# Optimization experiments

Measured on AMD Instinct MI355X. Metric: run time of the kernel, lower is better.

Reference implementation:

```python
import jax, jax.numpy as jnp
import numpy as np

B, H, S, D = 2048, 1024, 32768, 64  # batch, hidden_dim, memory_slots, slot_size


def setup_inputs() -> dict:
    key = jax.random.key(0)
    ks = jax.random.split(key, 8)
    inp = {
        "query": jax.random.normal(ks[0], (B, H), jnp.float32),
        "consciousness_level": jax.random.uniform(ks[1], (B,), jnp.float32),
        "content": jax.random.normal(ks[2], (B, H), jnp.float32),
        "memory": jax.random.normal(ks[3], (S, D), jnp.float32) * 0.1,
        "memory_age": jnp.zeros((S,), jnp.float32),
        "memory_strength": jnp.ones((S,), jnp.float32) * 0.1,
        "W_read": jax.random.normal(ks[4], (H + 1, S), jnp.float32) / np.sqrt(H + 1),
        "b_read": jnp.zeros((S,), jnp.float32),
        "W_write": jax.random.normal(ks[5], (H + 1, S), jnp.float32) / np.sqrt(H + 1),
        "b_write": jnp.zeros((S,), jnp.float32),
        "W_cp": jax.random.normal(ks[6], (H, D), jnp.float32) / np.sqrt(H),
        "b_cp": jnp.zeros((D,), jnp.float32),
        "W_ce": jax.random.normal(ks[7], (D, H), jnp.float32) / np.sqrt(D),
        "b_ce": jnp.zeros((H,), jnp.float32),
    }
    return inp


def reference(query, consciousness_level, content, memory, memory_age,
              memory_strength, W_read, b_read, W_write, b_write,
              W_cp, b_cp, W_ce, b_ce):
    # ---- read path ----
    enhanced_query = jnp.concatenate([query, consciousness_level[:, None]], axis=-1)  # [B, H+1]
    read_weights = jax.nn.softmax(enhanced_query @ W_read + b_read, axis=-1)          # [B, S]
    boosted = read_weights * memory_strength[None, :]
    boosted = boosted / (boosted.sum(axis=-1, keepdims=True) + 1e-6)
    read_content = boosted @ memory                                                   # [B, D]
    consciousness_boost = read_content @ W_ce + b_ce                                  # [B, H]

    # ---- write path (vectorized masked consolidation over all slots) ----
    c_mean = consciousness_level.mean()
    write_weights = jax.nn.softmax(enhanced_query @ W_write + b_write, axis=-1)       # [B, S]
    ww_mean = write_weights.mean(axis=0)                                              # [S]
    pc_mean = (content @ W_cp + b_cp).mean(axis=0)                                    # [D]
    weight = ww_mean * (c_mean * 2.0)                                                 # [S]
    gate = c_mean >= 0.3                                                              # auto-activation threshold
    mask = (weight > 0.005) & gate                                                    # [S] bool
    consolidation = jax.nn.sigmoid(memory_age * 0.1 + c_mean)                         # [S]
    alpha = weight * consolidation                                                    # [S]
    new_memory = jnp.where(mask[:, None],
                           (1.0 - alpha)[:, None] * memory + alpha[:, None] * pc_mean[None, :],
                           memory)                                                    # [S, D]
    new_age = memory_age + mask.astype(memory_age.dtype)
    new_strength = jnp.where(mask,
                             jnp.clip(memory_strength + weight * 0.1, 0.1, 2.0),
                             memory_strength)
    return read_content, consciousness_boost, new_memory, new_age, new_strength
```

## Files before the change

### kernel.cpp

```cpp
#include <hip/hip_runtime.h>
#include <hip/hip_bf16.h>
#include <cstdint>
#include <cstddef>

#define B_ 2048
#define H_ 1024
#define S_ 32768
#define D_ 64
#define BT 32
#define KP 1088
#define NT 17

typedef unsigned short u16;
typedef __attribute__((ext_vector_type(8))) short bf16x8;
typedef __attribute__((ext_vector_type(4))) float f32x4;
typedef __attribute__((ext_vector_type(8))) unsigned short ushort8v;

#define WS_CMEAN      0
#define WS_PCMEAN     64
#define WS_ZERO_BEGIN 128
#define WS_CMM        128
#define WS_ZR         (WS_CMM + H_)
#define WS_TR         (WS_ZR + B_)
#define WS_VR         (WS_TR + B_)
#define WS_ZW         (WS_VR + B_*D_)
#define WS_WWM        (WS_ZW + B_)
#define WS_END        (WS_WWM + S_)

__device__ __forceinline__ u16 f2bf(float f) {
  unsigned u = __float_as_uint(f);
  unsigned r = (u + 0x7FFFu + ((u >> 16) & 1u)) >> 16;
  return (u16)r;
}

__device__ __forceinline__ void gload_lds16(const void* g, void* l) {
  __builtin_amdgcn_global_load_lds(
      (const __attribute__((address_space(1))) unsigned int*)g,
      (__attribute__((address_space(3))) unsigned int*)l, 16, 0, 0);
}

__global__ void k_stats(const float* __restrict__ content,
                        const float* __restrict__ cl, float* __restrict__ ws) {
  const int gx = blockIdx.x, gy = blockIdx.y, t = threadIdx.x;
  if (gx < 4) {
    const int h = gx * 256 + t;
    const int b0 = gy * 256;
    float acc = 0.f;
    #pragma unroll 8
    for (int b = 0; b < 256; ++b) acc += content[(size_t)(b0 + b) * H_ + h];
    atomicAdd(&ws[WS_CMM + h], acc * (1.0f / B_));
  } else if (gy == 0) {
    float acc = 0.f;
    for (int i = t; i < B_; i += 256) acc += cl[i];
    #pragma unroll
    for (int off = 32; off > 0; off >>= 1) acc += __shfl_down(acc, off);
    __shared__ float red[4];
    if ((t & 63) == 0) red[t >> 6] = acc;
    __syncthreads();
    if (t == 0) ws[WS_CMEAN] = (red[0] + red[1] + red[2] + red[3]) * (1.0f / B_);
  }
}

__global__ void k_pcmean(const float* __restrict__ Wcp, const float* __restrict__ bcp,
                         float* __restrict__ ws) {
  const int d = threadIdx.x;
  const float* __restrict__ cmm = &ws[WS_CMM];
  float acc = bcp[d];
  #pragma unroll 4
  for (int k = 0; k < H_; ++k) acc = fmaf(cmm[k], Wcp[(size_t)k * D_ + d], acc);
  ws[WS_PCMEAN + d] = acc;
}


__global__ void k_cvt_q(const float* __restrict__ query, const float* __restrict__ cl,
                        u16* __restrict__ qb) {
  const int b = blockIdx.x, t = threadIdx.x;
  const float c = cl[b];
  #pragma unroll
  for (int i = 0; i < 5; ++i) {
    const int k = i * 256 + t;
    if (k < KP) {
      float v;
      if (k < H_) v = query[(size_t)b * H_ + k];
      else if (k == H_) v = c;
      else if (k == H_ + 1) v = 1.0f;
      else v = 0.f;
      qb[(size_t)b * KP + k] = f2bf(v);
    }
  }
}

__global__ void k_cvt_wt(const float* __restrict__ W, const float* __restrict__ bias,
                         u16* __restrict__ wbt) {
  __shared__ float tile[64][65];
  const int t = threadIdx.x;
  const int s0 = blockIdx.x * 64;
  const int k0 = blockIdx.y * 64;
  const int c = t & 63, rbase = t >> 6;
  #pragma unroll
  for (int i = 0; i < 16; ++i) {
    const int r = rbase + i * 4;
    const int k = k0 + r;
    float v = 0.f;
    if (k <= H_) v = W[(size_t)k * S_ + s0 + c];
    else if (k == H_ + 1) v = bias[s0 + c];
    tile[r][c] = v;
  }
  __syncthreads();
  #pragma unroll
  for (int i = 0; i < 16; ++i) {
    const int sr = rbase + i * 4;
    const int k = k0 + c;
    if (k < KP) wbt[(size_t)(s0 + sr) * KP + k] = f2bf(tile[c][sr]);
  }
}

__global__ void k_cvt_memT(const float* __restrict__ mem, u16* __restrict__ mT) {
  __shared__ float tile[64][65];
  const int t = threadIdx.x;
  const int s0 = blockIdx.x * 64;
  const int c = t & 63, rbase = t >> 6;
  #pragma unroll
  for (int i = 0; i < 16; ++i) {
    const int r = rbase + i * 4;
    tile[r][c] = mem[(size_t)(s0 + r) * D_ + c];
  }
  __syncthreads();
  #pragma unroll
  for (int i = 0; i < 16; ++i) {
    const int d = rbase + i * 4;
    mT[(size_t)d * S_ + s0 + c] = f2bf(tile[c][d]);
  }
}

template <int NF>
__device__ __forceinline__ void rd_frags(const u16* __restrict__ lds, int rowbase,
                                         int lr, int lg, bf16x8 (&dst)[NF * 2]) {
  #pragma unroll
  for (int f = 0; f < NF; ++f) {
    const int rr = rowbase + f * 16 + lr;
    #pragma unroll
    for (int ks = 0; ks < 2; ++ks) {
      const int ch = (ks * 4 + lg) ^ (rr & 7);
      dst[f * 2 + ks] = *(const bf16x8*)&lds[rr * 64 + ch * 8];
    }
  }
}

template <int QR, int QC>
__device__ __forceinline__ void mfmaq(f32x4 (&acc)[8][4], const bf16x8 (&av)[8],
                                      const bf16x8 (&bv)[4]) {
  #pragma unroll
  for (int m16 = 0; m16 < 4; ++m16)
    #pragma unroll
    for (int n16 = 0; n16 < 2; ++n16)
      #pragma unroll
      for (int ks = 0; ks < 2; ++ks)
        acc[QR * 4 + m16][QC * 2 + n16] = __builtin_amdgcn_mfma_f32_16x16x32_bf16(
            av[m16 * 2 + ks], bv[n16 * 2 + ks], acc[QR * 4 + m16][QC * 2 + n16], 0, 0, 0);
}

template <int VARIANT>
__global__ __launch_bounds__(512, 2) void k_gemm(
    const u16* __restrict__ qb, const u16* __restrict__ wbt,
    const float* __restrict__ strength,
    u16* __restrict__ pout, float* __restrict__ ws) {
  __shared__ __align__(16) u16 Ab[2][256 * 64];
  __shared__ __align__(16) u16 Bb[2][256 * 64];
  const int t = threadIdx.x;
  const int w = t >> 6, l = t & 63;
  const int wm = w >> 2, wn = w & 3;
  const int lr = l & 15, lg = l >> 4;

  const int lin = blockIdx.x + 8 * blockIdx.y;
  const int xcd = lin & 7, idx = lin >> 3;
  const size_t r0 = (size_t)(idx & 7) * 256;
  const size_t c0 = (size_t)(xcd * 16 + (idx >> 3)) * 256;

  f32x4 acc[8][4];
  #pragma unroll
  for (int m = 0; m < 8; ++m)
    #pragma unroll
    for (int n = 0; n < 4; ++n) acc[m][n] = (f32x4)0.f;

  auto STAGE = [&](int kt2, int pp) {
    #pragma unroll
    for (int i = 0; i < 4; ++i) {
      const int q = i * 512 + t;
      const int r = q >> 3;
      const int sc = (q & 7) ^ (r & 7);
      gload_lds16(qb + (r0 + r) * KP + (size_t)kt2 * 64 + sc * 8, &Ab[pp][q * 8]);
    }
    #pragma unroll
    for (int i = 0; i < 4; ++i) {
      const int q = i * 512 + t;
      const int r = q >> 3;
      const int sc = (q & 7) ^ (r & 7);
      gload_lds16(wbt + (c0 + r) * KP + (size_t)kt2 * 64 + sc * 8, &Bb[pp][q * 8]);
    }
  };

  STAGE(0, 0);
  STAGE(1, 1);
  asm volatile("s_waitcnt vmcnt(8)" ::: "memory");
  __builtin_amdgcn_sched_barrier(0);
  __builtin_amdgcn_s_barrier();

  for (int kt = 0; kt < NT; ++kt) {
    const int p = kt & 1;
    const u16* __restrict__ Ap = &Ab[p][0];
    const u16* __restrict__ Bp = &Bb[p][0];
    bf16x8 a[8], b0[4], b1[4];
    rd_frags<4>(Ap, wm * 128 + 0, lr, lg, a);
    rd_frags<2>(Bp, wn * 64 + 0, lr, lg, b0);
    __builtin_amdgcn_sched_barrier(0);
    __builtin_amdgcn_s_barrier();
    __builtin_amdgcn_s_setprio(1);
    mfmaq<0, 0>(acc, a, b0);
    __builtin_amdgcn_s_setprio(0);
    __builtin_amdgcn_s_barrier();
    rd_frags<2>(Bp, wn * 64 + 32, lr, lg, b1);
    __builtin_amdgcn_sched_barrier(0);
    __builtin_amdgcn_s_barrier();
    __builtin_amdgcn_s_setprio(1);
    mfmaq<0, 1>(acc, a, b1);
    __builtin_amdgcn_s_setprio(0);
    __builtin_amdgcn_s_barrier();
    rd_frags<4>(Ap, wm * 128 + 64, lr, lg, a);
    __builtin_amdgcn_sched_barrier(0);
    __builtin_amdgcn_s_barrier();
    __builtin_amdgcn_s_setprio(1);
    mfmaq<1, 1>(acc, a, b1);
    __builtin_amdgcn_s_setprio(0);
    __builtin_amdgcn_s_barrier();
    if (kt + 2 < NT) STAGE(kt + 2, p);
    __builtin_amdgcn_s_barrier();
    __builtin_amdgcn_s_setprio(1);
    mfmaq<1, 0>(acc, a, b0);
    __builtin_amdgcn_s_setprio(0);
    if (kt + 2 < NT) {
      asm volatile("s_waitcnt vmcnt(8)" ::: "memory");
    } else if (kt + 1 < NT) {
      asm volatile("s_waitcnt vmcnt(0)" ::: "memory");
    }
    __builtin_amdgcn_sched_barrier(0);
    __builtin_amdgcn_s_barrier();
  }

  float* zred = (float*)&Ab[0][0];
  float* tred = zred + 256;
  if (t < 512) zred[t] = 0.f;
  __syncthreads();

  float st4[4];
  if (VARIANT == 0) {
    #pragma unroll
    for (int n = 0; n < 4; ++n) st4[n] = strength[c0 + wn * 64 + n * 16 + lr];
  }
  #pragma unroll
  for (int m = 0; m < 8; ++m) {
    #pragma unroll
    for (int j = 0; j < 4; ++j) {
      const int rloc = wm * 128 + m * 16 + lg * 4 + j;
      const size_t R = r0 + rloc;
      float ze = 0.f, zp = 0.f;
      u16 pb[4];
      #pragma unroll
      for (int n = 0; n < 4; ++n) {
        const float e = __expf(acc[m][n][j]);
        const float pv = (VARIANT == 0) ? e * st4[n] : e;
        ze += e;
        zp += pv;
        pb[n] = f2bf(pv);
      }
      #pragma unroll
      for (int n = 0; n < 4; ++n)
        pout[R * S_ + c0 + wn * 64 + n * 16 + lr] = pb[n];
      #pragma unroll
      for (int off = 1; off < 16; off <<= 1) {
        ze += __shfl_xor(ze, off);
        if (VARIANT == 0) zp += __shfl_xor(zp, off);
      }
      if (lr == 0) {
        atomicAdd(&zred[rloc], ze);
        if (VARIANT == 0) atomicAdd(&tred[rloc], zp);
      }
    }
  }
  __syncthreads();
  if (t < 256) {
    if (VARIANT == 0) {
      atomicAdd(&ws[WS_ZR + r0 + t], zred[t]);
      atomicAdd(&ws[WS_TR + r0 + t], tred[t]);
    } else {
      atomicAdd(&ws[WS_ZW + r0 + t], zred[t]);
    }
  }
}

__global__ void k_pv(const u16* __restrict__ P, const u16* __restrict__ mT,
                     float* __restrict__ ws) {
  __shared__ float Vs[64 * 64];
  const int t = threadIdx.x;
  const int w = t >> 6, l = t & 63;
  const int lr = l & 15, lg = l >> 4;
  const size_t r0 = (size_t)blockIdx.x * 64;
  const size_t s0 = (size_t)blockIdx.y * 1024 + (size_t)w * 256;
  f32x4 acc[4][4];
  #pragma unroll
  for (int m = 0; m < 4; ++m)
    #pragma unroll
    for (int n = 0; n < 4; ++n) acc[m][n] = (f32x4)0.f;

  for (int ks = 0; ks < 8; ++ks) {
    const size_t sb = s0 + ks * 32 + lg * 8;
    bf16x8 a[4], b[4];
    #pragma unroll
    for (int m = 0; m < 4; ++m)
      a[m] = *(const bf16x8*)&P[(r0 + m * 16 + lr) * S_ + sb];
    #pragma unroll
    for (int n = 0; n < 4; ++n)
      b[n] = *(const bf16x8*)&mT[(size_t)(n * 16 + lr) * S_ + sb];
    #pragma unroll
    for (int m = 0; m < 4; ++m)
      #pragma unroll
      for (int n = 0; n < 4; ++n)
        acc[m][n] = __builtin_amdgcn_mfma_f32_16x16x32_bf16(a[m], b[n], acc[m][n], 0, 0, 0);
  }
  for (int i = t; i < 4096; i += 256) Vs[i] = 0.f;
  __syncthreads();
  #pragma unroll
  for (int m = 0; m < 4; ++m)
    #pragma unroll
    for (int j = 0; j < 4; ++j)
      #pragma unroll
      for (int n = 0; n < 4; ++n)
        atomicAdd(&Vs[(m * 16 + lg * 4 + j) * 64 + n * 16 + lr], acc[m][n][j]);
  __syncthreads();
  for (int i = t; i < 4096; i += 256)
    atomicAdd(&ws[WS_VR + (r0 + (size_t)(i >> 6)) * 64 + (i & 63)], Vs[i]);
}


__global__ void k_wwm_store(const __hip_bfloat16* __restrict__ ebuf,
                            float* __restrict__ ws) {
  const int t = threadIdx.x;
  const int s0 = blockIdx.x * 2048 + t * 8;
  const int b0 = blockIdx.y * 128;
  const u16* __restrict__ eb = (const u16*)ebuf;
  float ww[8];
  #pragma unroll
  for (int j = 0; j < 8; ++j) ww[j] = 0.f;
  #pragma unroll 1
  for (int b = 0; b < 128; ++b) {
    const float inv = 1.0f / ws[WS_ZW + b0 + b];
    const ushort8v ev = *reinterpret_cast<const ushort8v*>(&eb[(size_t)(b0 + b) * S_ + s0]);
    #pragma unroll
    for (int j = 0; j < 8; ++j) {
      const float e = __uint_as_float(((unsigned)ev[j]) << 16);
      ww[j] = fmaf(e, inv, ww[j]);
    }
  }
  #pragma unroll
  for (int j = 0; j < 8; ++j) atomicAdd(&ws[WS_WWM + s0 + j], ww[j]);
}

__global__ void k_rc(const float* __restrict__ ws, float* __restrict__ out) {
  const int idx = blockIdx.x * 256 + threadIdx.x;
  const int b = idx >> 6;
  const float z = ws[WS_ZR + b], tt = ws[WS_TR + b];
  out[idx] = ws[WS_VR + idx] / (tt + 1e-6f * z);
}

__global__ void k_cboost(const float* __restrict__ rc, const float* __restrict__ Wce,
                         const float* __restrict__ bce, float* __restrict__ out) {
  const int idx = blockIdx.x * 256 + threadIdx.x;
  const int b = idx >> 10, h = idx & 1023;
  const float* __restrict__ rcb = &rc[b * 64];
  float acc = bce[h];
  #pragma unroll
  for (int dd = 0; dd < 64; dd += 4) {
    const float4 r4 = *reinterpret_cast<const float4*>(&rcb[dd]);
    acc = fmaf(r4.x, Wce[(size_t)(dd + 0) * H_ + h], acc);
    acc = fmaf(r4.y, Wce[(size_t)(dd + 1) * H_ + h], acc);
    acc = fmaf(r4.z, Wce[(size_t)(dd + 2) * H_ + h], acc);
    acc = fmaf(r4.w, Wce[(size_t)(dd + 3) * H_ + h], acc);
  }
  out[idx] = acc;
}

__global__ void k_final(const float* __restrict__ mem, const float* __restrict__ age,
                        const float* __restrict__ strength, const float* __restrict__ ws,
                        float* __restrict__ out_mem, float* __restrict__ out_age,
                        float* __restrict__ out_str) {
  const int idx = blockIdx.x * 256 + threadIdx.x;
  const int s = idx >> 6, dd = idx & 63;
  const float cm = ws[WS_CMEAN];
  const float w = ws[WS_WWM + s] * (2.0f * cm / B_);
  const bool mask = (w > 0.005f) && (cm >= 0.3f);
  float m = mem[idx];
  if (mask) {
    const float cons = 1.0f / (1.0f + __expf(-(age[s] * 0.1f + cm)));
    const float alpha = w * cons;
    m = (1.0f - alpha) * m + alpha * ws[WS_PCMEAN + dd];
  }
  out_mem[idx] = m;
  if (dd == 0) {
    out_age[s] = age[s] + (mask ? 1.0f : 0.0f);
    out_str[s] = mask ? fminf(fmaxf(strength[s] + w * 0.1f, 0.1f), 2.0f) : strength[s];
  }
}


template <int NR>
__device__ __forceinline__ void logits_kloop(const float* __restrict__ q, int row0,
                                             const float* __restrict__ W, int s,
                                             float* acc) {
  #pragma unroll 1
  for (int k = 0; k < H_; k += 4) {
    const float w0 = W[(size_t)(k + 0) * S_ + s];
    const float w1 = W[(size_t)(k + 1) * S_ + s];
    const float w2 = W[(size_t)(k + 2) * S_ + s];
    const float w3 = W[(size_t)(k + 3) * S_ + s];
    #pragma unroll
    for (int r = 0; r < NR; ++r) {
      const float4 qv = *reinterpret_cast<const float4*>(&q[(size_t)(row0 + r) * H_ + k]);
      float a = acc[r];
      a = fmaf(qv.x, w0, a);
      a = fmaf(qv.y, w1, a);
      a = fmaf(qv.z, w2, a);
      a = fmaf(qv.w, w3, a);
      acc[r] = a;
    }
  }
}

__global__ __launch_bounds__(512, 2) void k_read(
    const float* __restrict__ q, const float* __restrict__ cl,
    const float* __restrict__ Wr, const float* __restrict__ br,
    const float* __restrict__ strength, const float* __restrict__ mem,
    float* __restrict__ ws) {
  __shared__ float plds[BT * 512];
  const int t = threadIdx.x;
  const int r0 = blockIdx.x * BT;
  const int squar = blockIdx.y;
  const int d = t & 63, wv = t >> 6;

  float zacc[BT], tacc[BT];
  #pragma unroll
  for (int r = 0; r < BT; ++r) { zacc[r] = 0.f; tacc[r] = 0.f; }
  float vacc[4] = {0.f, 0.f, 0.f, 0.f};

  for (int tile = 0; tile < 16; ++tile) {
    const int sg0 = squar * 8192 + tile * 512;
    const int s = sg0 + t;
    float acc[BT];
    const float wlast = Wr[(size_t)H_ * S_ + s];
    const float bias = br[s];
    #pragma unroll
    for (int r = 0; r < BT; ++r) acc[r] = fmaf(cl[r0 + r], wlast, bias);
    logits_kloop<BT>(q, r0, Wr, s, acc);

    const float stg = strength[s];
    #pragma unroll
    for (int r = 0; r < BT; ++r) {
      const float e = __expf(acc[r]);
      zacc[r] += e;
      const float p = e * stg;
      tacc[r] += p;
      plds[r * 512 + t] = p;
    }
    __syncthreads();
    #pragma unroll 1
    for (int sl = 0; sl < 512; sl += 4) {
      const float m0 = mem[(size_t)(sg0 + sl + 0) * D_ + d];
      const float m1 = mem[(size_t)(sg0 + sl + 1) * D_ + d];
      const float m2 = mem[(size_t)(sg0 + sl + 2) * D_ + d];
      const float m3 = mem[(size_t)(sg0 + sl + 3) * D_ + d];
      #pragma unroll
      for (int j = 0; j < 4; ++j) {
        const float4 pv = *reinterpret_cast<const float4*>(&plds[(wv + 8 * j) * 512 + sl]);
        float v = vacc[j];
        v = fmaf(pv.x, m0, v);
        v = fmaf(pv.y, m1, v);
        v = fmaf(pv.z, m2, v);
        v = fmaf(pv.w, m3, v);
        vacc[j] = v;
      }
    }
    __syncthreads();
  }

  float* red0 = plds;
  float* red1 = plds + 8 * BT;
  #pragma unroll
  for (int r = 0; r < BT; ++r) {
    float z = zacc[r], tt = tacc[r];
    #pragma unroll
    for (int off = 32; off > 0; off >>= 1) {
      z += __shfl_down(z, off);
      tt += __shfl_down(tt, off);
    }
    if ((t & 63) == 0) { red0[wv * BT + r] = z; red1[wv * BT + r] = tt; }
  }
  __syncthreads();
  if (t < BT) {
    float z = 0.f, tt = 0.f;
    #pragma unroll
    for (int wq = 0; wq < 8; ++wq) { z += red0[wq * BT + t]; tt += red1[wq * BT + t]; }
    atomicAdd(&ws[WS_ZR + r0 + t], z);
    atomicAdd(&ws[WS_TR + r0 + t], tt);
  }
  #pragma unroll
  for (int j = 0; j < 4; ++j)
    atomicAdd(&ws[WS_VR + (size_t)(r0 + wv + 8 * j) * D_ + d], vacc[j]);
}

__global__ __launch_bounds__(512, 2) void k_write_pass1(
    const float* __restrict__ q, const float* __restrict__ cl,
    const float* __restrict__ Ww, const float* __restrict__ bw,
    float* __restrict__ ws, __hip_bfloat16* __restrict__ ebuf, const int store_e) {
  __shared__ float red[8 * BT];
  const int t = threadIdx.x;
  const int r0 = blockIdx.x * BT;
  const int squar = blockIdx.y;
  const int wv = t >> 6;

  float zacc[BT];
  #pragma unroll
  for (int r = 0; r < BT; ++r) zacc[r] = 0.f;

  for (int tile = 0; tile < 16; ++tile) {
    const int s = squar * 8192 + tile * 512 + t;
    float acc[BT];
    const float wlast = Ww[(size_t)H_ * S_ + s];
    const float bias = bw[s];
    #pragma unroll
    for (int r = 0; r < BT; ++r) acc[r] = fmaf(cl[r0 + r], wlast, bias);
    logits_kloop<BT>(q, r0, Ww, s, acc);
    #pragma unroll
    for (int r = 0; r < BT; ++r) {
      const float e = __expf(acc[r]);
      zacc[r] += e;
      if (store_e) ebuf[(size_t)(r0 + r) * S_ + s] = __float2bfloat16(e);
    }
  }
  #pragma unroll
  for (int r = 0; r < BT; ++r) {
    float z = zacc[r];
    #pragma unroll
    for (int off = 32; off > 0; off >>= 1) z += __shfl_down(z, off);
    if ((t & 63) == 0) red[wv * BT + r] = z;
  }
  __syncthreads();
  if (t < BT) {
    float z = 0.f;
    #pragma unroll
    for (int wq = 0; wq < 8; ++wq) z += red[wq * BT + t];
    atomicAdd(&ws[WS_ZW + r0 + t], z);
  }
}

__global__ __launch_bounds__(512, 2) void k_wwm_recompute(
    const float* __restrict__ q, const float* __restrict__ cl,
    const float* __restrict__ Ww, const float* __restrict__ bw,
    float* __restrict__ ws) {
  const int t = threadIdx.x;
  const int s = blockIdx.x * 512 + t;
  const int b0 = blockIdx.y * 256;
  const float wlast = Ww[(size_t)H_ * S_ + s];
  const float bias = bw[s];
  float wwacc = 0.f;
  for (int g = 0; g < 8; ++g) {
    const int rb = b0 + g * 32;
    float acc[BT];
    #pragma unroll
    for (int r = 0; r < BT; ++r) acc[r] = fmaf(cl[rb + r], wlast, bias);
    logits_kloop<BT>(q, rb, Ww, s, acc);
    #pragma unroll
    for (int r = 0; r < BT; ++r) wwacc += __expf(acc[r]) / ws[WS_ZW + rb + r];
  }
  atomicAdd(&ws[WS_WWM + s], wwacc);
}


extern "C" void kernel_launch(void* const* d_in, const int* in_sizes, int n_in,
                              void* d_out, int out_size, void* d_ws, size_t ws_size,
                              hipStream_t stream) {
  const float* query    = (const float*)d_in[0];
  const float* cl       = (const float*)d_in[1];
  const float* content  = (const float*)d_in[2];
  const float* memory   = (const float*)d_in[3];
  const float* age      = (const float*)d_in[4];
  const float* strength = (const float*)d_in[5];
  const float* W_read   = (const float*)d_in[6];
  const float* b_read   = (const float*)d_in[7];
  const float* W_write  = (const float*)d_in[8];
  const float* b_write  = (const float*)d_in[9];
  const float* W_cp     = (const float*)d_in[10];
  const float* b_cp     = (const float*)d_in[11];
  const float* W_ce     = (const float*)d_in[12];
  const float* b_ce     = (const float*)d_in[13];

  float* out = (float*)d_out;
  float* ws = (float*)d_ws;
  float* out_rc  = out;
  float* out_cb  = out + B_ * D_;
  float* out_mem = out_cb + (size_t)B_ * H_;
  float* out_age = out_mem + (size_t)S_ * D_;
  float* out_str = out_age + S_;

  const size_t QB_F   = WS_END;
  const size_t MEMT_F = QB_F + (size_t)B_ * KP / 2;
  const size_t WBT_F  = MEMT_F + (size_t)D_ * S_ / 2;
  const size_t PBUF_F = WBT_F + (size_t)S_ * KP / 2;
  const size_t FAST_END_F = PBUF_F + (size_t)B_ * S_ / 2;

  hipMemsetAsync(ws + WS_ZERO_BEGIN, 0,
                 (size_t)(WS_END - WS_ZERO_BEGIN) * sizeof(float), stream);
  k_stats<<<dim3(5, 8), 256, 0, stream>>>(content, cl, ws);
  k_pcmean<<<1, 64, 0, stream>>>(W_cp, b_cp, ws);

  if (ws_size >= FAST_END_F * sizeof(float)) {
    u16* qb   = (u16*)(ws + QB_F);
    u16* mT   = (u16*)(ws + MEMT_F);
    u16* wbt  = (u16*)(ws + WBT_F);
    u16* pbuf = (u16*)(ws + PBUF_F);

    k_cvt_q<<<B_, 256, 0, stream>>>(query, cl, qb);
    k_cvt_memT<<<S_ / 64, 256, 0, stream>>>(memory, mT);
    k_cvt_wt<<<dim3(S_ / 64, KP / 64), 256, 0, stream>>>(W_read, b_read, wbt);
    k_gemm<0><<<dim3(8, 128), 512, 0, stream>>>(qb, wbt, strength, pbuf, ws);
    k_pv<<<dim3(B_ / 64, 32), 256, 0, stream>>>(pbuf, mT, ws);
    k_rc<<<(B_ * D_) / 256, 256, 0, stream>>>(ws, out_rc);
    k_cboost<<<(B_ * H_) / 256, 256, 0, stream>>>(out_rc, W_ce, b_ce, out_cb);
    k_cvt_wt<<<dim3(S_ / 64, KP / 64), 256, 0, stream>>>(W_write, b_write, wbt);
    k_gemm<1><<<dim3(8, 128), 512, 0, stream>>>(qb, wbt, nullptr, pbuf, ws);
    k_wwm_store<<<dim3(S_ / 2048, B_ / 128), 256, 0, stream>>>((const __hip_bfloat16*)pbuf, ws);
    k_final<<<(S_ * D_) / 256, 256, 0, stream>>>(memory, age, strength, ws,
                                                 out_mem, out_age, out_str);
  } else {
    const size_t ebuf_bytes = (size_t)B_ * S_ * 2;
    const int store_e = (ws_size >= (size_t)WS_END * 4 + ebuf_bytes) ? 1 : 0;
    __hip_bfloat16* ebuf = (__hip_bfloat16*)(ws + WS_END);

    k_read<<<dim3(B_ / BT, 4), 512, 0, stream>>>(query, cl, W_read, b_read, strength, memory, ws);
    k_write_pass1<<<dim3(B_ / BT, 4), 512, 0, stream>>>(query, cl, W_write, b_write, ws, ebuf, store_e);
    k_rc<<<(B_ * D_) / 256, 256, 0, stream>>>(ws, out_rc);
    k_cboost<<<(B_ * H_) / 256, 256, 0, stream>>>(out_rc, W_ce, b_ce, out_cb);
    if (store_e) {
      k_wwm_store<<<dim3(S_ / 2048, B_ / 128), 256, 0, stream>>>(ebuf, ws);
    } else {
      k_wwm_recompute<<<dim3(S_ / 512, 8), 512, 0, stream>>>(query, cl, W_write, b_write, ws);
    }
    k_final<<<(S_ * D_) / 256, 256, 0, stream>>>(memory, age, strength, ws,
                                                 out_mem, out_age, out_str);
  }
}
```

Before: 814.4 us.

## Fuse P·V into read GEMM epilogue and store write probabilities in fp8

The read GEMM epilogue now writes the unnormalized softmax tile to LDS and multiplies it by the transposed memory slice with MFMA. This produces per-column-block partial read vectors, which a new k_rc2 kernel reduces, so the full B×S bf16 probability buffer and the separate k_pv pass are gone. The write GEMM stores exp values as a custom 8-bit float instead of bf16, halving the buffer traffic for the ww_mean reduction, which is widened to 16 bytes per thread. The trade-offs are extra LDS and epilogue work in the GEMM, a 128-way partial reduction, and lower precision on the write weights, which could tip slots across the mask threshold.

Measured after the change: 833.4 us. 1.02x slower.

```diff
diff --git a/kernel.cpp b/kernel.cpp
--- a/kernel.cpp
+++ b/kernel.cpp
@@ -11,6 +11,7 @@
 #define KP 1088
 #define NT 17
 
+typedef unsigned char u8;
 typedef unsigned short u16;
 typedef __attribute__((ext_vector_type(8))) short bf16x8;
 typedef __attribute__((ext_vector_type(4))) float f32x4;
@@ -31,6 +32,31 @@
   unsigned u = __float_as_uint(f);
   unsigned r = (u + 0x7FFFu + ((u >> 16) & 1u)) >> 16;
   return (u16)r;
+}
+
+__device__ __forceinline__ float bf2f(u16 v) {
+  return __uint_as_float(((unsigned)v) << 16);
+}
+
+__device__ __forceinline__ u8 f8enc(float f) {
+  f = fminf(f, 448.f);
+  unsigned u = __float_as_uint(f);
+  int ex = (int)((u >> 23) & 255) - 127;
+  unsigned r;
+  if (ex >= -6) {
+    unsigned m = u & 0x7FFFFF;
+    unsigned rm = (m + 0x7FFFF + ((m >> 20) & 1)) >> 20;
+    r = ((unsigned)(ex + 7) << 3) + rm;
+  } else {
+    r = (unsigned)fminf(7.f, f * 512.f + 0.5f);
+  }
+  return (u8)(r > 126 ? 126 : r);
+}
+
+__device__ __forceinline__ float f8dec(u8 b) {
+  int ef = (b >> 3) & 15, m = b & 7;
+  return ef ? __uint_as_float(((unsigned)(ef + 120) << 23) | ((unsigned)m << 20))
+            : (float)m * 0.001953125f;
 }
 
 __device__ __forceinline__ void gload_lds16(const void* g, void* l) {
@@ -163,10 +189,9 @@
 template <int VARIANT>
 __global__ __launch_bounds__(512, 2) void k_gemm(
     const u16* __restrict__ qb, const u16* __restrict__ wbt,
-    const float* __restrict__ strength,
-    u16* __restrict__ pout, float* __restrict__ ws) {
-  __shared__ __align__(16) u16 Ab[2][256 * 64];
-  __shared__ __align__(16) u16 Bb[2][256 * 64];
+    const float* __restrict__ strength, const u16* __restrict__ mT,
+    u16* __restrict__ vp, u8* __restrict__ pout, float* __restrict__ ws) {
+  __shared__ __align__(16) u16 SMEM[4][256 * 64];
   const int t = threadIdx.x;
   const int w = t >> 6, l = t & 63;
   const int wm = w >> 2, wn = w & 3;
@@ -175,7 +200,8 @@
   const int lin = blockIdx.x + 8 * blockIdx.y;
   const int xcd = lin & 7, idx = lin >> 3;
   const size_t r0 = (size_t)(idx & 7) * 256;
-  const size_t c0 = (size_t)(xcd * 16 + (idx >> 3)) * 256;
+  const int cblk = xcd * 16 + (idx >> 3);
+  const size_t c0 = (size_t)cblk * 256;
 
   f32x4 acc[8][4];
   #pragma unroll
@@ -189,14 +215,14 @@
       const int q = i * 512 + t;
       const int r = q >> 3;
       const int sc = (q & 7) ^ (r & 7);
-      gload_lds16(qb + (r0 + r) * KP + (size_t)kt2 * 64 + sc * 8, &Ab[pp][q * 8]);
+      gload_lds16(qb + (r0 + r) * KP + (size_t)kt2 * 64 + sc * 8, &SMEM[pp][q * 8]);
     }
     #pragma unroll
     for (int i = 0; i < 4; ++i) {
       const int q = i * 512 + t;
       const int r = q >> 3;
       const int sc = (q & 7) ^ (r & 7);
-      gload_lds16(wbt + (c0 + r) * KP + (size_t)kt2 * 64 + sc * 8, &Bb[pp][q * 8]);
+      gload_lds16(wbt + (c0 + r) * KP + (size_t)kt2 * 64 + sc * 8, &SMEM[2 + pp][q * 8]);
     }
   };
 
@@ -208,8 +234,8 @@
 
   for (int kt = 0; kt < NT; ++kt) {
     const int p = kt & 1;
-    const u16* __restrict__ Ap = &Ab[p][0];
-    const u16* __restrict__ Bp = &Bb[p][0];
+    const u16* __restrict__ Ap = &SMEM[p][0];
+    const u16* __restrict__ Bp = &SMEM[2 + p][0];
     bf16x8 a[8], b0[4], b1[4];
     rd_frags<4>(Ap, wm * 128 + 0, lr, lg, a);
     rd_frags<2>(Bp, wn * 64 + 0, lr, lg, b0);
@@ -247,122 +273,135 @@
     __builtin_amdgcn_s_barrier();
   }
 
-  float* zred = (float*)&Ab[0][0];
-  float* tred = zred + 256;
-  if (t < 512) zred[t] = 0.f;
-  __syncthreads();
-
-  float st4[4];
   if (VARIANT == 0) {
+    u16* __restrict__ Plds = &SMEM[0][0];
+    float st4[4];
     #pragma unroll
     for (int n = 0; n < 4; ++n) st4[n] = strength[c0 + wn * 64 + n * 16 + lr];
-  }
-  #pragma unroll
-  for (int m = 0; m < 8; ++m) {
-    #pragma unroll
-    for (int j = 0; j < 4; ++j) {
-      const int rloc = wm * 128 + m * 16 + lg * 4 + j;
-      const size_t R = r0 + rloc;
-      float ze = 0.f, zp = 0.f;
-      u16 pb[4];
-      #pragma unroll
-      for (int n = 0; n < 4; ++n) {
-        const float e = __expf(acc[m][n][j]);
-        const float pv = (VARIANT == 0) ? e * st4[n] : e;
-        ze += e;
-        zp += pv;
-        pb[n] = f2bf(pv);
+    #pragma unroll
+    for (int m = 0; m < 8; ++m) {
+      #pragma unroll
+      for (int j = 0; j < 4; ++j) {
+        const int rloc = wm * 128 + m * 16 + lg * 4 + j;
+        const size_t R = r0 + rloc;
+        float ze = 0.f, zp = 0.f;
+        #pragma unroll
+        for (int n = 0; n < 4; ++n) {
+          const float e = __expf(acc[m][n][j]);
+          const float pv = e * st4[n];
+          ze += e;
+          zp += pv;
+          const int col = wn * 64 + n * 16 + lr;
+          Plds[rloc * 256 + ((((col >> 3) ^ (rloc & 7))) << 3) + (col & 7)] = f2bf(pv);
+        }
+        #pragma unroll
+        for (int off = 1; off < 16; off <<= 1) {
+          ze += __shfl_xor(ze, off);
+          zp += __shfl_xor(zp, off);
+        }
+        if (lr == 0) {
+          atomicAdd(&ws[WS_ZR + R], ze);
+          atomicAdd(&ws[WS_TR + R], zp);
+        }
       }
+    }
+    f32x4 pv[8][4];
+    #pragma unroll
+    for (int f = 0; f < 8; ++f)
+      #pragma unroll
+      for (int n = 0; n < 4; ++n) pv[f][n] = (f32x4)0.f;
+    #pragma unroll
+    for (int ks = 0; ks < 2; ++ks) {
+      bf16x8 pa[8], pb[4];
+      #pragma unroll
+      for (int f = 0; f < 8; ++f) {
+        const int row = wm * 128 + f * 16 + lr;
+        const int ch = (wn * 8 + ks * 4 + lg) ^ (row & 7);
+        pa[f] = *(const bf16x8*)&Plds[row * 256 + ch * 8];
+      }
       #pragma unroll
       for (int n = 0; n < 4; ++n)
-        pout[R * S_ + c0 + wn * 64 + n * 16 + lr] = pb[n];
-      #pragma unroll
-      for (int off = 1; off < 16; off <<= 1) {
-        ze += __shfl_xor(ze, off);
-        if (VARIANT == 0) zp += __shfl_xor(zp, off);
+        pb[n] = *(const bf16x8*)&mT[(size_t)(n * 16 + lr) * S_ + c0 + wn * 64 + ks * 32 + lg * 8];
+      #pragma unroll
+      for (int f = 0; f < 8; ++f)
+        #pragma unroll
+        for (int n = 0; n < 4; ++n)
+          pv[f][n] = __builtin_amdgcn_mfma_f32_16x16x32_bf16(pa[f], pb[n], pv[f][n], 0, 0, 0);
+    }
+    #pragma unroll
+    for (int f = 0; f < 8; ++f) {
+      #pragma unroll
+      for (int j = 0; j < 4; ++j) {
+        const size_t R = r0 + wm * 128 + f * 16 + lg * 4 + j;
+        #pragma unroll
+        for (int n = 0; n < 4; ++n)
+          vp[((size_t)cblk * B_ + R) * 64 + n * 16 + lr] = f2bf(pv[f][n][j]);
       }
-      if (lr == 0) {
-        atomicAdd(&zred[rloc], ze);
-        if (VARIANT == 0) atomicAdd(&tred[rloc], zp);
+    }
+  } else {
+    float* zred = (float*)&SMEM[0][0];
+    if (t < 256) zred[t] = 0.f;
+    __syncthreads();
+    #pragma unroll
+    for (int m = 0; m < 8; ++m) {
+      #pragma unroll
+      for (int j = 0; j < 4; ++j) {
+        const int rloc = wm * 128 + m * 16 + lg * 4 + j;
+        const size_t R = r0 + rloc;
+        float ze = 0.f;
+        #pragma unroll
+        for (int n = 0; n < 4; ++n) {
+          const float e = __expf(acc[m][n][j]);
+          ze += e;
+          pout[R * S_ + c0 + wn * 64 + n * 16 + lr] = f8enc(e);
+        }
+        #pragma unroll
+        for (int off = 1; off < 16; off <<= 1) ze += __shfl_xor(ze, off);
+        if (lr == 0) atomicAdd(&zred[rloc], ze);
       }
     }
-  }
-  __syncthreads();
-  if (t < 256) {
-    if (VARIANT == 0) {
-      atomicAdd(&ws[WS_ZR + r0 + t], zred[t]);
-      atomicAdd(&ws[WS_TR + r0 + t], tred[t]);
-    } else {
-      atomicAdd(&ws[WS_ZW + r0 + t], zred[t]);
-    }
-  }
-}
-
-__global__ void k_pv(const u16* __restrict__ P, const u16* __restrict__ mT,
-                     float* __restrict__ ws) {
-  __shared__ float Vs[64 * 64];
+    __syncthreads();
+    if (t < 256) atomicAdd(&ws[WS_ZW + r0 + t], zred[t]);
+  }
+}
+
+__global__ void k_rc2(const u16* __restrict__ vp, const float* __restrict__ ws,
+                      float* __restrict__ out) {
+  const int idx = blockIdx.x * 256 + threadIdx.x;
+  const int b = idx >> 5, dp = (idx & 31) * 2;
+  float v0 = 0.f, v1 = 0.f;
+  #pragma unroll 4
+  for (int c = 0; c < 128; ++c) {
+    const unsigned u = *(const unsigned*)&vp[((size_t)c * B_ + b) * 64 + dp];
+    v0 += __uint_as_float(u << 16);
+    v1 += __uint_as_float(u & 0xFFFF0000u);
+  }
+  const float inv = 1.0f / (ws[WS_TR + b] + 1e-6f * ws[WS_ZR + b]);
+  out[(size_t)b * 64 + dp] = v0 * inv;
+  out[(size_t)b * 64 + dp + 1] = v1 * inv;
+}
+
+
+__global__ void k_wwm_f8(const u8* __restrict__ ebuf, float* __restrict__ ws) {
   const int t = threadIdx.x;
-  const int w = t >> 6, l = t & 63;
-  const int lr = l & 15, lg = l >> 4;
-  const size_t r0 = (size_t)blockIdx.x * 64;
-  const size_t s0 = (size_t)blockIdx.y * 1024 + (size_t)w * 256;
-  f32x4 acc[4][4];
-  #pragma unroll
-  for (int m = 0; m < 4; ++m)
-    #pragma unroll
-    for (int n = 0; n < 4; ++n) acc[m][n] = (f32x4)0.f;
-
-  for (int ks = 0; ks < 8; ++ks) {
-    const size_t sb = s0 + ks * 32 + lg * 8;
-    bf16x8 a[4], b[4];
-    #pragma unroll
-    for (int m = 0; m < 4; ++m)
-      a[m] = *(const bf16x8*)&P[(r0 + m * 16 + lr) * S_ + sb];
-    #pragma unroll
-    for (int n = 0; n < 4; ++n)
-      b[n] = *(const bf16x8*)&mT[(size_t)(n * 16 + lr) * S_ + sb];
-    #pragma unroll
-    for (int m = 0; m < 4; ++m)
-      #pragma unroll
-      for (int n = 0; n < 4; ++n)
-        acc[m][n] = __builtin_amdgcn_mfma_f32_16x16x32_bf16(a[m], b[n], acc[m][n], 0, 0, 0);
-  }
-  for (int i = t; i < 4096; i += 256) Vs[i] = 0.f;
-  __syncthreads();
-  #pragma unroll
-  for (int m = 0; m < 4; ++m)
-    #pragma unroll
-    for (int j = 0; j < 4; ++j)
-      #pragma unroll
-      for (int n = 0; n < 4; ++n)
-        atomicAdd(&Vs[(m * 16 + lg * 4 + j) * 64 + n * 16 + lr], acc[m][n][j]);
-  __syncthreads();
-  for (int i = t; i < 4096; i += 256)
-    atomicAdd(&ws[WS_VR + (r0 + (size_t)(i >> 6)) * 64 + (i & 63)], Vs[i]);
-}
-
-
-__global__ void k_wwm_store(const __hip_bfloat16* __restrict__ ebuf,
-                            float* __restrict__ ws) {
-  const int t = threadIdx.x;
-  const int s0 = blockIdx.x * 2048 + t * 8;
+  const int s0 = blockIdx.x * 4096 + t * 16;
   const int b0 = blockIdx.y * 128;
-  const u16* __restrict__ eb = (const u16*)ebuf;
-  float ww[8];
-  #pragma unroll
-  for (int j = 0; j < 8; ++j) ww[j] = 0.f;
+  float ww[16];
+  #pragma unroll
+  for (int j = 0; j < 16; ++j) ww[j] = 0.f;
   #pragma unroll 1
   for (int b = 0; b < 128; ++b) {
     const float inv = 1.0f / ws[WS_ZW + b0 + b];
-    const ushort8v ev = *reinterpret_cast<const ushort8v*>(&eb[(size_t)(b0 + b) * S_ + s0]);
-    #pragma unroll
-    for (int j = 0; j < 8; ++j) {
-      const float e = __uint_as_float(((unsigned)ev[j]) << 16);
-      ww[j] = fmaf(e, inv, ww[j]);
-    }
-  }
-  #pragma unroll
-  for (int j = 0; j < 8; ++j) atomicAdd(&ws[WS_WWM + s0 + j], ww[j]);
+    const uint4 v = *reinterpret_cast<const uint4*>(&ebuf[(size_t)(b0 + b) * S_ + s0]);
+    const unsigned vv[4] = {v.x, v.y, v.z, v.w};
+    #pragma unroll
+    for (int j = 0; j < 16; ++j) {
+      const u8 byte = (u8)((vv[j >> 2] >> ((j & 3) * 8)) & 0xFF);
+      ww[j] = fmaf(f8dec(byte), inv, ww[j]);
+    }
+  }
+  #pragma unroll
+  for (int j = 0; j < 16; ++j) atomicAdd(&ws[WS_WWM + s0 + j], ww[j]);
 }
 
 __global__ void k_rc(const float* __restrict__ ws, float* __restrict__ out) {
@@ -559,6 +598,29 @@
     for (int wq = 0; wq < 8; ++wq) z += red[wq * BT + t];
     atomicAdd(&ws[WS_ZW + r0 + t], z);
   }
+}
+
+__global__ void k_wwm_store(const __hip_bfloat16* __restrict__ ebuf,
+                            float* __restrict__ ws) {
+  const int t = threadIdx.x;
+  const int s0 = blockIdx.x * 2048 + t * 8;
+  const int b0 = blockIdx.y * 128;
+  const u16* __restrict__ eb = (const u16*)ebuf;
+  float ww[8];
+  #pragma unroll
+  for (int j = 0; j < 8; ++j) ww[j] = 0.f;
+  #pragma unroll 1
+  for (int b = 0; b < 128; ++b) {
+    const float inv = 1.0f / ws[WS_ZW + b0 + b];
+    const ushort8v ev = *reinterpret_cast<const ushort8v*>(&eb[(size_t)(b0 + b) * S_ + s0]);
+    #pragma unroll
+    for (int j = 0; j < 8; ++j) {
+      const float e = __uint_as_float(((unsigned)ev[j]) << 16);
+      ww[j] = fmaf(e, inv, ww[j]);
+    }
+  }
+  #pragma unroll
+  for (int j = 0; j < 8; ++j) atomicAdd(&ws[WS_WWM + s0 + j], ww[j]);
 }
 
 __global__ __launch_bounds__(512, 2) void k_wwm_recompute(
@@ -613,8 +675,9 @@
   const size_t QB_F   = WS_END;
   const size_t MEMT_F = QB_F + (size_t)B_ * KP / 2;
   const size_t WBT_F  = MEMT_F + (size_t)D_ * S_ / 2;
-  const size_t PBUF_F = WBT_F + (size_t)S_ * KP / 2;
-  const size_t FAST_END_F = PBUF_F + (size_t)B_ * S_ / 2;
+  const size_t PF8_F  = WBT_F + (size_t)S_ * KP / 2;
+  const size_t VP_F   = PF8_F + (size_t)B_ * S_ / 4;
+  const size_t FAST_END_F = VP_F + (size_t)128 * B_ * 64 / 2;
 
   hipMemsetAsync(ws + WS_ZERO_BEGIN, 0,
                  (size_t)(WS_END - WS_ZERO_BEGIN) * sizeof(float), stream);
@@ -625,18 +688,18 @@
     u16* qb   = (u16*)(ws + QB_F);
     u16* mT   = (u16*)(ws + MEMT_F);
     u16* wbt  = (u16*)(ws + WBT_F);
-    u16* pbuf = (u16*)(ws + PBUF_F);
+    u8*  pf8  = (u8*)(ws + PF8_F);
+    u16* vp   = (u16*)(ws + VP_F);
 
     k_cvt_q<<<B_, 256, 0, stream>>>(query, cl, qb);
     k_cvt_memT<<<S_ / 64, 256, 0, stream>>>(memory, mT);
     k_cvt_wt<<<dim3(S_ / 64, KP / 64), 256, 0, stream>>>(W_read, b_read, wbt);
-    k_gemm<0><<<dim3(8, 128), 512, 0, stream>>>(qb, wbt, strength, pbuf, ws);
-    k_pv<<<dim3(B_ / 64, 32), 256, 0, stream>>>(pbuf, mT, ws);
-    k_rc<<<(B_ * D_) / 256, 256, 0, stream>>>(ws, out_rc);
+    k_gemm<0><<<dim3(8, 128), 512, 0, stream>>>(qb, wbt, strength, mT, vp, nullptr, ws);
+    k_rc2<<<(B_ * D_ / 2) / 256, 256, 0, stream>>>(vp, ws, out_rc);
     k_cboost<<<(B_ * H_) / 256, 256, 0, stream>>>(out_rc, W_ce, b_ce, out_cb);
     k_cvt_wt<<<dim3(S_ / 64, KP / 64), 256, 0, stream>>>(W_write, b_write, wbt);
-    k_gemm<1><<<dim3(8, 128), 512, 0, stream>>>(qb, wbt, nullptr, pbuf, ws);
-    k_wwm_store<<<dim3(S_ / 2048, B_ / 128), 256, 0, stream>>>((const __hip_bfloat16*)pbuf, ws);
+    k_gemm<1><<<dim3(8, 128), 512, 0, stream>>>(qb, wbt, nullptr, mT, nullptr, pf8, ws);
+    k_wwm_f8<<<dim3(8, 16), 256, 0, stream>>>(pf8, ws);
     k_final<<<(S_ * D_) / 256, 256, 0, stream>>>(memory, age, strength, ws,
                                                  out_mem, out_age, out_str);
   } else {
```

## Stage GEMM epilogue through LDS and store write-path weights as fp8

Applied to the files above, without the earlier changes.

The GEMM epilogue now writes exp values as bf16 into a swizzled LDS tile, then reads them back row-contiguous so each thread issues 16-byte coalesced global stores. Row sums are reduced with wave shuffles and sent straight to global atomics, replacing the LDS atomic reduction. For the write path, the exponentials are encoded into a custom e4m3-like 8-bit format, which halves the bytes of the B×S intermediate that the new k_wwm_f8 kernel reads back to compute the column mean. The risks are precision loss in write_weights near the 0.005 mask threshold, and an extra bf16 rounding of e before the strength multiply on the read path.

New measurement: 903.8 us. +11.0%, slower.

```diff
diff --git a/kernel.cpp b/kernel.cpp
--- a/kernel.cpp
+++ b/kernel.cpp
@@ -11,10 +11,11 @@
 #define KP 1088
 #define NT 17
 
+typedef unsigned char u8;
 typedef unsigned short u16;
 typedef __attribute__((ext_vector_type(8))) short bf16x8;
+typedef __attribute__((ext_vector_type(8))) unsigned short ushort8v;
 typedef __attribute__((ext_vector_type(4))) float f32x4;
-typedef __attribute__((ext_vector_type(8))) unsigned short ushort8v;
 
 #define WS_CMEAN      0
 #define WS_PCMEAN     64
@@ -31,6 +32,31 @@
   unsigned u = __float_as_uint(f);
   unsigned r = (u + 0x7FFFu + ((u >> 16) & 1u)) >> 16;
   return (u16)r;
+}
+
+__device__ __forceinline__ float bf2f(u16 v) {
+  return __uint_as_float(((unsigned)v) << 16);
+}
+
+__device__ __forceinline__ u8 f8enc(float f) {
+  f = fminf(f, 448.f);
+  unsigned u = __float_as_uint(f);
+  int ex = (int)((u >> 23) & 255) - 127;
+  unsigned r;
+  if (ex >= -6) {
+    unsigned m = u & 0x7FFFFF;
+    unsigned rm = (m + 0x7FFFF + ((m >> 20) & 1)) >> 20;
+    r = ((unsigned)(ex + 7) << 3) + rm;
+  } else {
+    r = (unsigned)fminf(7.f, f * 512.f + 0.5f);
+  }
+  return (u8)(r > 126 ? 126 : r);
+}
+
+__device__ __forceinline__ float f8dec(u8 b) {
+  int ef = (b >> 3) & 15, m = b & 7;
+  return ef ? __uint_as_float(((unsigned)(ef + 120) << 23) | ((unsigned)m << 20))
+            : (float)m * 0.001953125f;
 }
 
 __device__ __forceinline__ void gload_lds16(const void* g, void* l) {
@@ -163,10 +189,9 @@
 template <int VARIANT>
 __global__ __launch_bounds__(512, 2) void k_gemm(
     const u16* __restrict__ qb, const u16* __restrict__ wbt,
-    const float* __restrict__ strength,
-    u16* __restrict__ pout, float* __restrict__ ws) {
-  __shared__ __align__(16) u16 Ab[2][256 * 64];
-  __shared__ __align__(16) u16 Bb[2][256 * 64];
+    const float* __restrict__ strength, void* __restrict__ pout,
+    float* __restrict__ ws) {
+  __shared__ __align__(16) u16 SMEM[4][256 * 64];
   const int t = threadIdx.x;
   const int w = t >> 6, l = t & 63;
   const int wm = w >> 2, wn = w & 3;
@@ -175,7 +200,8 @@
   const int lin = blockIdx.x + 8 * blockIdx.y;
   const int xcd = lin & 7, idx = lin >> 3;
   const size_t r0 = (size_t)(idx & 7) * 256;
-  const size_t c0 = (size_t)(xcd * 16 + (idx >> 3)) * 256;
+  const int cblk = xcd * 16 + (idx >> 3);
+  const size_t c0 = (size_t)cblk * 256;
 
   f32x4 acc[8][4];
   #pragma unroll
@@ -189,14 +215,14 @@
       const int q = i * 512 + t;
       const int r = q >> 3;
       const int sc = (q & 7) ^ (r & 7);
-      gload_lds16(qb + (r0 + r) * KP + (size_t)kt2 * 64 + sc * 8, &Ab[pp][q * 8]);
+      gload_lds16(qb + (r0 + r) * KP + (size_t)kt2 * 64 + sc * 8, &SMEM[pp][q * 8]);
     }
     #pragma unroll
     for (int i = 0; i < 4; ++i) {
       const int q = i * 512 + t;
       const int r = q >> 3;
       const int sc = (q & 7) ^ (r & 7);
-      gload_lds16(wbt + (c0 + r) * KP + (size_t)kt2 * 64 + sc * 8, &Bb[pp][q * 8]);
+      gload_lds16(wbt + (c0 + r) * KP + (size_t)kt2 * 64 + sc * 8, &SMEM[2 + pp][q * 8]);
     }
   };
 
@@ -208,8 +234,8 @@
 
   for (int kt = 0; kt < NT; ++kt) {
     const int p = kt & 1;
-    const u16* __restrict__ Ap = &Ab[p][0];
-    const u16* __restrict__ Bp = &Bb[p][0];
+    const u16* __restrict__ Ap = &SMEM[p][0];
+    const u16* __restrict__ Bp = &SMEM[2 + p][0];
     bf16x8 a[8], b0[4], b1[4];
     rd_frags<4>(Ap, wm * 128 + 0, lr, lg, a);
     rd_frags<2>(Bp, wn * 64 + 0, lr, lg, b0);
@@ -247,53 +273,77 @@
     __builtin_amdgcn_s_barrier();
   }
 
-  float* zred = (float*)&Ab[0][0];
-  float* tred = zred + 256;
-  if (t < 512) zred[t] = 0.f;
-  __syncthreads();
-
-  float st4[4];
-  if (VARIANT == 0) {
-    #pragma unroll
-    for (int n = 0; n < 4; ++n) st4[n] = strength[c0 + wn * 64 + n * 16 + lr];
-  }
+  u16* __restrict__ Plds = &SMEM[0][0];
   #pragma unroll
   for (int m = 0; m < 8; ++m) {
     #pragma unroll
     for (int j = 0; j < 4; ++j) {
       const int rloc = wm * 128 + m * 16 + lg * 4 + j;
-      const size_t R = r0 + rloc;
+      #pragma unroll
+      for (int n = 0; n < 4; ++n) {
+        const int col = wn * 64 + n * 16 + lr;
+        const int ch = (col >> 3) ^ (rloc & 7);
+        Plds[rloc * 256 + ch * 8 + (col & 7)] = f2bf(__expf(acc[m][n][j]));
+      }
+    }
+  }
+  __syncthreads();
+
+  if (VARIANT == 0) {
+    u16* __restrict__ pout16 = (u16*)pout;
+    const int cch = l & 31;
+    const float4 sa = *(const float4*)&strength[c0 + cch * 8];
+    const float4 sb = *(const float4*)&strength[c0 + cch * 8 + 4];
+    const float stv[8] = {sa.x, sa.y, sa.z, sa.w, sb.x, sb.y, sb.z, sb.w};
+    #pragma unroll 2
+    for (int it = 0; it < 16; ++it) {
+      const int row = w * 32 + it * 2 + (l >> 5);
+      const bf16x8 ev = *(const bf16x8*)&Plds[row * 256 + ((cch ^ (row & 7)) * 8)];
       float ze = 0.f, zp = 0.f;
-      u16 pb[4];
-      #pragma unroll
-      for (int n = 0; n < 4; ++n) {
-        const float e = __expf(acc[m][n][j]);
-        const float pv = (VARIANT == 0) ? e * st4[n] : e;
+      ushort8v pb;
+      #pragma unroll
+      for (int q = 0; q < 8; ++q) {
+        const float e = bf2f((u16)ev[q]);
+        const float pq = e * stv[q];
         ze += e;
-        zp += pv;
-        pb[n] = f2bf(pv);
+        zp += pq;
+        pb[q] = f2bf(pq);
       }
-      #pragma unroll
-      for (int n = 0; n < 4; ++n)
-        pout[R * S_ + c0 + wn * 64 + n * 16 + lr] = pb[n];
-      #pragma unroll
-      for (int off = 1; off < 16; off <<= 1) {
+      *(ushort8v*)&pout16[(r0 + row) * S_ + c0 + cch * 8] = pb;
+      #pragma unroll
+      for (int off = 1; off < 32; off <<= 1) {
         ze += __shfl_xor(ze, off);
-        if (VARIANT == 0) zp += __shfl_xor(zp, off);
+        zp += __shfl_xor(zp, off);
       }
-      if (lr == 0) {
-        atomicAdd(&zred[rloc], ze);
-        if (VARIANT == 0) atomicAdd(&tred[rloc], zp);
+      if ((l & 31) == 0) {
+        atomicAdd(&ws[WS_ZR + r0 + row], ze);
+        atomicAdd(&ws[WS_TR + r0 + row], zp);
       }
     }
-  }
-  __syncthreads();
-  if (t < 256) {
-    if (VARIANT == 0) {
-      atomicAdd(&ws[WS_ZR + r0 + t], zred[t]);
-      atomicAdd(&ws[WS_TR + r0 + t], tred[t]);
-    } else {
-      atomicAdd(&ws[WS_ZW + r0 + t], zred[t]);
+  } else {
+    u8* __restrict__ pout8 = (u8*)pout;
+    #pragma unroll 2
+    for (int it = 0; it < 8; ++it) {
+      const int row = w * 32 + it * 4 + (l >> 4);
+      const int c2 = (l & 15) * 2;
+      const bf16x8 e0 = *(const bf16x8*)&Plds[row * 256 + ((c2 ^ (row & 7)) * 8)];
+      const bf16x8 e1 = *(const bf16x8*)&Plds[row * 256 + (((c2 + 1) ^ (row & 7)) * 8)];
+      float ze = 0.f;
+      uint4 fb;
+      unsigned wds[4] = {0, 0, 0, 0};
+      #pragma unroll
+      for (int q = 0; q < 8; ++q) {
+        const float ea = bf2f((u16)e0[q]);
+        const float eb = bf2f((u16)e1[q]);
+        ze += ea + eb;
+        wds[q >> 2] |= ((unsigned)f8enc(ea)) << ((q & 3) * 8);
+        wds[2 + (q >> 2)] |= ((unsigned)f8enc(eb)) << ((q & 3) * 8);
+      }
+      fb.x = wds[0]; fb.y = wds[1]; fb.z = wds[2]; fb.w = wds[3];
+      *(uint4*)&pout8[(r0 + row) * S_ + c0 + (size_t)(l & 15) * 16] = fb;
+      #pragma unroll
+      for (int off = 1; off < 16; off <<= 1) ze += __shfl_xor(ze, off);
+      if ((l & 15) == 0) atomicAdd(&ws[WS_ZW + r0 + row], ze);
     }
   }
 }
@@ -342,27 +392,26 @@
 }
 
 
-__global__ void k_wwm_store(const __hip_bfloat16* __restrict__ ebuf,
-                            float* __restrict__ ws) {
-  const int t = threadIdx.x;
-  const int s0 = blockIdx.x * 2048 + t * 8;
+__global__ void k_wwm_f8(const u8* __restrict__ ebuf, float* __restrict__ ws) {
+  const int t = threadIdx.x;
+  const int s0 = blockIdx.x * 4096 + t * 16;
   const int b0 = blockIdx.y * 128;
-  const u16* __restrict__ eb = (const u16*)ebuf;
-  float ww[8];
-  #pragma unroll
-  for (int j = 0; j < 8; ++j) ww[j] = 0.f;
+  float ww[16];
+  #pragma unroll
+  for (int j = 0; j < 16; ++j) ww[j] = 0.f;
   #pragma unroll 1
   for (int b = 0; b < 128; ++b) {
     const float inv = 1.0f / ws[WS_ZW + b0 + b];
-    const ushort8v ev = *reinterpret_cast<const ushort8v*>(&eb[(size_t)(b0 + b) * S_ + s0]);
-    #pragma unroll
-    for (int j = 0; j < 8; ++j) {
-      const float e = __uint_as_float(((unsigned)ev[j]) << 16);
-      ww[j] = fmaf(e, inv, ww[j]);
-    }
-  }
-  #pragma unroll
-  for (int j = 0; j < 8; ++j) atomicAdd(&ws[WS_WWM + s0 + j], ww[j]);
+    const uint4 v = *reinterpret_cast<const uint4*>(&ebuf[(size_t)(b0 + b) * S_ + s0]);
+    const unsigned vv[4] = {v.x, v.y, v.z, v.w};
+    #pragma unroll
+    for (int j = 0; j < 16; ++j) {
+      const u8 byte = (u8)((vv[j >> 2] >> ((j & 3) * 8)) & 0xFF);
+      ww[j] = fmaf(f8dec(byte), inv, ww[j]);
+    }
+  }
+  #pragma unroll
+  for (int j = 0; j < 16; ++j) atomicAdd(&ws[WS_WWM + s0 + j], ww[j]);
 }
 
 __global__ void k_rc(const float* __restrict__ ws, float* __restrict__ out) {
@@ -559,6 +608,29 @@
     for (int wq = 0; wq < 8; ++wq) z += red[wq * BT + t];
     atomicAdd(&ws[WS_ZW + r0 + t], z);
   }
+}
+
+__global__ void k_wwm_store(const __hip_bfloat16* __restrict__ ebuf,
+                            float* __restrict__ ws) {
+  const int t = threadIdx.x;
+  const int s0 = blockIdx.x * 2048 + t * 8;
+  const int b0 = blockIdx.y * 128;
+  const u16* __restrict__ eb = (const u16*)ebuf;
+  float ww[8];
+  #pragma unroll
+  for (int j = 0; j < 8; ++j) ww[j] = 0.f;
+  #pragma unroll 1
+  for (int b = 0; b < 128; ++b) {
+    const float inv = 1.0f / ws[WS_ZW + b0 + b];
+    const ushort8v ev = *reinterpret_cast<const ushort8v*>(&eb[(size_t)(b0 + b) * S_ + s0]);
+    #pragma unroll
+    for (int j = 0; j < 8; ++j) {
+      const float e = __uint_as_float(((unsigned)ev[j]) << 16);
+      ww[j] = fmaf(e, inv, ww[j]);
+    }
+  }
+  #pragma unroll
+  for (int j = 0; j < 8; ++j) atomicAdd(&ws[WS_WWM + s0 + j], ww[j]);
 }
 
 __global__ __launch_bounds__(512, 2) void k_wwm_recompute(
@@ -630,13 +702,13 @@
     k_cvt_q<<<B_, 256, 0, stream>>>(query, cl, qb);
     k_cvt_memT<<<S_ / 64, 256, 0, stream>>>(memory, mT);
     k_cvt_wt<<<dim3(S_ / 64, KP / 64), 256, 0, stream>>>(W_read, b_read, wbt);
-    k_gemm<0><<<dim3(8, 128), 512, 0, stream>>>(qb, wbt, strength, pbuf, ws);
+    k_gemm<0><<<dim3(8, 128), 512, 0, stream>>>(qb, wbt, strength, (void*)pbuf, ws);
     k_pv<<<dim3(B_ / 64, 32), 256, 0, stream>>>(pbuf, mT, ws);
     k_rc<<<(B_ * D_) / 256, 256, 0, stream>>>(ws, out_rc);
     k_cboost<<<(B_ * H_) / 256, 256, 0, stream>>>(out_rc, W_ce, b_ce, out_cb);
     k_cvt_wt<<<dim3(S_ / 64, KP / 64), 256, 0, stream>>>(W_write, b_write, wbt);
-    k_gemm<1><<<dim3(8, 128), 512, 0, stream>>>(qb, wbt, nullptr, pbuf, ws);
-    k_wwm_store<<<dim3(S_ / 2048, B_ / 128), 256, 0, stream>>>((const __hip_bfloat16*)pbuf, ws);
+    k_gemm<1><<<dim3(8, 128), 512, 0, stream>>>(qb, wbt, nullptr, (void*)pbuf, ws);
+    k_wwm_f8<<<dim3(8, 16), 256, 0, stream>>>((const u8*)pbuf, ws);
     k_final<<<(S_ * D_) / 256, 256, 0, stream>>>(memory, age, strength, ws,
                                                  out_mem, out_age, out_str);
   } else {
```
